# Kernel optimization log

Hardware: AMD Instinct MI355X
Metric: run time of the kernel (lower is better)

The kernel has to match this reference:

```python
import jax, jax.numpy as jnp
import numpy as np

SCALING = 16.0 / 8.0  # lora_alpha / r


def setup_inputs() -> dict:
    key = jax.random.key(0)
    k1, k2, k3, k4 = jax.random.split(key, 4)
    B, S, D_IN, D_OUT, R = 4, 4096, 4096, 4096, 8
    x = jax.random.normal(k1, (B, S, D_IN), dtype=jnp.float32)
    weight = jax.random.normal(k2, (D_OUT, D_IN), dtype=jnp.float32) * 0.02
    lora_A = jax.random.normal(k3, (R, D_IN), dtype=jnp.float32) * 0.02
    lora_B = jax.random.normal(k4, (D_OUT, R), dtype=jnp.float32) * 0.02
    return {"x": x, "weight": weight, "lora_A": lora_A, "lora_B": lora_B}


def reference(x, weight, lora_A, lora_B):
    # Base frozen linear: x @ W^T   (bias='none')
    base = jnp.einsum('bsd,od->bso', x, weight)
    # LoRA path (dropout in eval mode = identity):
    # down-project to rank r, up-project to out, scale, residual-add.
    lora_low = jnp.einsum('bsd,rd->bsr', x, lora_A)      # [B,S,r]
    lora_out = jnp.einsum('bsr,or->bso', lora_low, lora_B)  # [B,S,out]
    return base + lora_out * SCALING
```

## Files before the change

### kernel.cpp

```cpp
#include <hip/hip_runtime.h>
#include <hip/hip_bf16.h>


typedef __bf16 bf16;
typedef bf16 bf16x8 __attribute__((ext_vector_type(8)));
typedef float f32x4 __attribute__((ext_vector_type(4)));

typedef __attribute__((address_space(1))) const void* as1cv;
typedef __attribute__((address_space(3))) void* as3v;

constexpr int Mdim = 16384;
constexpr int Ndim = 4096;
constexpr int Kdim = 4096;
constexpr int Rdim = 8;
constexpr float kScale = 2.0f;

__device__ __forceinline__ unsigned short f2bf(float f) {
  union { float f; unsigned u; } v; v.f = f;
  unsigned u = v.u;
  u += 0x7fffu + ((u >> 16) & 1u);
  return (unsigned short)(u >> 16);
}

__global__ void cast_x_kernel(const float4* __restrict__ x4,
                              ushort4* __restrict__ o4, int n4) {
  int i = blockIdx.x * blockDim.x + threadIdx.x;
  int stride = gridDim.x * blockDim.x;
  for (; i < n4; i += stride) {
    float4 v = x4[i];
    ushort4 o;
    o.x = f2bf(v.x); o.y = f2bf(v.y); o.z = f2bf(v.z); o.w = f2bf(v.w);
    o4[i] = o;
  }
}

__global__ void make_weff_kernel(const float* __restrict__ W,
                                 const float* __restrict__ A,
                                 const float* __restrict__ Bm,
                                 ushort* __restrict__ weff) {
  int tid = blockIdx.x * blockDim.x + threadIdx.x;
  int kc = tid & 511;
  int n = tid >> 9;
  if (n >= Ndim) return;

  const float* wp = W + (long)n * Kdim + kc * 8;
  float4 w0 = *(const float4*)(wp);
  float4 w1 = *(const float4*)(wp + 4);

  float4 b0 = *(const float4*)(Bm + n * Rdim);
  float4 b1 = *(const float4*)(Bm + n * Rdim + 4);
  float bs[8] = {b0.x, b0.y, b0.z, b0.w, b1.x, b1.y, b1.z, b1.w};

  float l[8] = {0.f, 0.f, 0.f, 0.f, 0.f, 0.f, 0.f, 0.f};
#pragma unroll
  for (int r = 0; r < Rdim; ++r) {
    const float* ap = A + (long)r * Kdim + kc * 8;
    float4 a0 = *(const float4*)(ap);
    float4 a1 = *(const float4*)(ap + 4);
    l[0] += bs[r] * a0.x; l[1] += bs[r] * a0.y;
    l[2] += bs[r] * a0.z; l[3] += bs[r] * a0.w;
    l[4] += bs[r] * a1.x; l[5] += bs[r] * a1.y;
    l[6] += bs[r] * a1.z; l[7] += bs[r] * a1.w;
  }

  float o[8] = {w0.x + kScale * l[0], w0.y + kScale * l[1],
                w0.z + kScale * l[2], w0.w + kScale * l[3],
                w1.x + kScale * l[4], w1.y + kScale * l[5],
                w1.z + kScale * l[6], w1.w + kScale * l[7]};
  uint4 pk;
  pk.x = (unsigned)f2bf(o[0]) | ((unsigned)f2bf(o[1]) << 16);
  pk.y = (unsigned)f2bf(o[2]) | ((unsigned)f2bf(o[3]) << 16);
  pk.z = (unsigned)f2bf(o[4]) | ((unsigned)f2bf(o[5]) << 16);
  pk.w = (unsigned)f2bf(o[6]) | ((unsigned)f2bf(o[7]) << 16);
  *(uint4*)(weff + (long)n * Kdim + kc * 8) = pk;
}

#define BM 256
#define BN 256
#define BK 64
#define NT (Kdim / BK)

#define SCHED0 __builtin_amdgcn_sched_barrier(0)
#define BAR do { SCHED0; __builtin_amdgcn_s_barrier(); SCHED0; } while (0)
#define VMCNT(n) do { asm volatile("s_waitcnt vmcnt(" #n ")" ::: "memory"); SCHED0; } while (0)
#define LGKM(n) do { asm volatile("s_waitcnt lgkmcnt(" #n ")" ::: "memory"); SCHED0; } while (0)
#define GLOAD(src, dst) \
  __builtin_amdgcn_global_load_lds((as1cv)(src), (as3v)(dst), 16, 0, 0)


__global__ __launch_bounds__(512, 2) void gemm256(const bf16* __restrict__ Xb,
                                                  const bf16* __restrict__ Wb,
                                                  float* __restrict__ C) {
  __shared__ bf16 lds[2][2][2][128 * 64];

  const int tid = threadIdx.x;
  const int lane = tid & 63;
  const int wave = tid >> 6;
  const int wr = wave >> 2;
  const int wc = wave & 3;
  const int fr = lane & 15;
  const int fq = lane >> 4;

  const int wg = blockIdx.x;
  const int swz = (wg & 7) * 128 + (wg >> 3);
  const int by = swz >> 4;
  const int bx = swz & 15;
  const int brow = by * BM;
  const int bcol = bx * BN;

  const int sLow = tid >> 3;
  const int cg = (tid & 7) ^ (sLow & 7);
  const bf16* pA = Xb + (long)(brow + sLow) * Kdim + cg * 8;
  const bf16* pB =
      Wb + (long)(bcol + (sLow & 31) + (sLow >> 5) * 64) * Kdim + cg * 8;

#define STAGE_A(buf, h, kt) do {                                              \
    const bf16* s_ = pA + (long)((h) * 64) * Kdim + (((kt) & (NT - 1)) * 64); \
    GLOAD(s_, &lds[buf][0][h][0] + tid * 8);                                  \
    GLOAD(s_ + (long)128 * Kdim, &lds[buf][0][h][4096] + tid * 8);            \
  } while (0)
#define STAGE_B(buf, h, kt) do {                                              \
    const bf16* s_ = pB + (long)((h) * 32) * Kdim + (((kt) & (NT - 1)) * 64); \
    GLOAD(s_, &lds[buf][1][h][0] + tid * 8);                                  \
    GLOAD(s_ + (long)128 * Kdim, &lds[buf][1][h][4096] + tid * 8);            \
  } while (0)

  const bf16* aBs[2] = {&lds[0][0][0][(wr * 64 + fr) * 64],
                        &lds[1][0][0][(wr * 64 + fr) * 64]};
  const bf16* bBs[2] = {&lds[0][1][0][(wc * 32 + fr) * 64],
                        &lds[1][1][0][(wc * 32 + fr) * 64]};
  const int cofs0 = ((fq + 0) ^ (fr & 7)) * 8;
  const int cofs1 = ((fq + 4) ^ (fr & 7)) * 8;

  f32x4 acc[8][4];
#pragma unroll
  for (int m = 0; m < 8; ++m)
#pragma unroll
    for (int n = 0; n < 4; ++n)
      acc[m][n] = (f32x4){0.f, 0.f, 0.f, 0.f};

  bf16x8 aF[4][2];
  bf16x8 bF[2][2][2];

#define LDA(buf, mh)                                                          \
  { _Pragma("unroll") for (int m4 = 0; m4 < 4; ++m4) {                        \
      aF[m4][0] = *(const bf16x8*)(aBs[buf] + (mh) * 8192 + m4 * 1024 + cofs0); \
      aF[m4][1] = *(const bf16x8*)(aBs[buf] + (mh) * 8192 + m4 * 1024 + cofs1); \
  } }
#define LDB(buf, nh)                                                          \
  { _Pragma("unroll") for (int n2 = 0; n2 < 2; ++n2) {                        \
      bF[nh][n2][0] = *(const bf16x8*)(bBs[buf] + (nh) * 8192 + n2 * 1024 + cofs0); \
      bF[nh][n2][1] = *(const bf16x8*)(bBs[buf] + (nh) * 8192 + n2 * 1024 + cofs1); \
  } }
#define MFMAQ(mh, nh)                                                         \
  { __builtin_amdgcn_s_setprio(1);                                            \
    _Pragma("unroll") for (int m4 = 0; m4 < 4; ++m4)                          \
    _Pragma("unroll") for (int n2 = 0; n2 < 2; ++n2)                          \
    _Pragma("unroll") for (int kk = 0; kk < 2; ++kk)                          \
      acc[(mh) * 4 + m4][(nh) * 2 + n2] =                                     \
          __builtin_amdgcn_mfma_f32_16x16x32_bf16(                            \
              aF[m4][kk], bF[nh][n2][kk], acc[(mh) * 4 + m4][(nh) * 2 + n2],  \
              0, 0, 0);                                                       \
    __builtin_amdgcn_s_setprio(0); }

#define TILE(bc, bn, t) do {                                                  \
                                                                      \
    STAGE_A(bn, 1, (t) + 1);                                                  \
    LDB(bc, 1);                                                               \
    BAR; LGKM(4);                                                             \
    MFMAQ(0, 0); BAR;                                                         \
                                                                      \
    STAGE_A(bc, 0, (t) + 2);                                                  \
    BAR; LGKM(0);                                                             \
    MFMAQ(0, 1); BAR;                                                         \
                                                                      \
    LDA(bc, 1);                                                               \
    STAGE_B(bc, 0, (t) + 2);                                                  \
    BAR; LGKM(0);                                                             \
    MFMAQ(1, 1);                                                              \
    VMCNT(6); BAR;                                                            \
                                                                      \
    MFMAQ(1, 0);                                                              \
    LDA(bn, 0);                                                               \
    LDB(bn, 0);                                                               \
    STAGE_B(bc, 1, (t) + 2);                                                  \
    VMCNT(6); BAR;                                                            \
  } while (0)

  STAGE_A(0, 0, 0); STAGE_B(0, 0, 0); STAGE_B(0, 1, 0); STAGE_A(0, 1, 0);
  STAGE_A(1, 0, 1); STAGE_B(1, 0, 1); STAGE_B(1, 1, 1);
  VMCNT(6); BAR;
  LDA(0, 0);
  LDB(0, 0);

#pragma unroll 1
  for (int t = 0; t < NT; t += 2) {
    TILE(0, 1, t);
    TILE(1, 0, t + 1);
  }
  VMCNT(0);

  const int crow = brow + wr * 128 + fq * 4;
  const int ccol = bcol + wc * 64 + fr;
#pragma unroll
  for (int m = 0; m < 8; ++m) {
#pragma unroll
    for (int n = 0; n < 4; ++n) {
      f32x4 v = acc[m][n];
      long base = (long)(crow + m * 16) * Ndim + (ccol + n * 16);
      C[base] = v[0];
      C[base + Ndim] = v[1];
      C[base + 2 * (long)Ndim] = v[2];
      C[base + 3 * (long)Ndim] = v[3];
    }
  }
}

extern "C" void kernel_launch(void* const* d_in, const int* in_sizes, int n_in,
                              void* d_out, int out_size, void* d_ws,
                              size_t ws_size, hipStream_t stream) {
  const float* x = (const float*)d_in[0];
  const float* W = (const float*)d_in[1];
  const float* lA = (const float*)d_in[2];
  const float* lB = (const float*)d_in[3];
  float* out = (float*)d_out;

  ushort* xb = (ushort*)d_ws;
  ushort* weff = xb + (size_t)Mdim * Kdim;

  cast_x_kernel<<<2048, 256, 0, stream>>>((const float4*)x, (ushort4*)xb,
                                          (Mdim * Kdim) / 4);
  make_weff_kernel<<<(Ndim * (Kdim / 8)) / 256, 256, 0, stream>>>(W, lA, lB,
                                                                  weff);
  dim3 grid((Mdim / BM) * (Ndim / BN));
  gemm256<<<grid, 512, 0, stream>>>((const bf16*)xb, (const bf16*)weff, out);
}
```

Measured before the change: 564.8 us.

## Double-buffer A fragments in registers and relax scheduling barriers

```diff
diff --git a/kernel.cpp b/kernel.cpp
--- a/kernel.cpp
+++ b/kernel.cpp
@@ -81,8 +81,8 @@
 #define NT (Kdim / BK)
 
 #define SCHED0 __builtin_amdgcn_sched_barrier(0)
-#define BAR do { SCHED0; __builtin_amdgcn_s_barrier(); SCHED0; } while (0)
-#define VMCNT(n) do { asm volatile("s_waitcnt vmcnt(" #n ")" ::: "memory"); SCHED0; } while (0)
+#define BAR __builtin_amdgcn_s_barrier()
+#define VMCNT(n) asm volatile("s_waitcnt vmcnt(" #n ")" ::: "memory")
 #define LGKM(n) do { asm volatile("s_waitcnt lgkmcnt(" #n ")" ::: "memory"); SCHED0; } while (0)
 #define GLOAD(src, dst) \
   __builtin_amdgcn_global_load_lds((as1cv)(src), (as3v)(dst), 16, 0, 0)
@@ -139,27 +139,28 @@
     for (int n = 0; n < 4; ++n)
       acc[m][n] = (f32x4){0.f, 0.f, 0.f, 0.f};
 
-  bf16x8 aF[4][2];
+  bf16x8 aF0[4][2];
+  bf16x8 aF1[4][2];
   bf16x8 bF[2][2][2];
 
-#define LDA(buf, mh)                                                          \
+#define LDA(dst, buf, mh)                                                     \
   { _Pragma("unroll") for (int m4 = 0; m4 < 4; ++m4) {                        \
-      aF[m4][0] = *(const bf16x8*)(aBs[buf] + (mh) * 8192 + m4 * 1024 + cofs0); \
-      aF[m4][1] = *(const bf16x8*)(aBs[buf] + (mh) * 8192 + m4 * 1024 + cofs1); \
+      dst[m4][0] = *(const bf16x8*)(aBs[buf] + (mh) * 8192 + m4 * 1024 + cofs0); \
+      dst[m4][1] = *(const bf16x8*)(aBs[buf] + (mh) * 8192 + m4 * 1024 + cofs1); \
   } }
 #define LDB(buf, nh)                                                          \
   { _Pragma("unroll") for (int n2 = 0; n2 < 2; ++n2) {                        \
       bF[nh][n2][0] = *(const bf16x8*)(bBs[buf] + (nh) * 8192 + n2 * 1024 + cofs0); \
       bF[nh][n2][1] = *(const bf16x8*)(bBs[buf] + (nh) * 8192 + n2 * 1024 + cofs1); \
   } }
-#define MFMAQ(mh, nh)                                                         \
+#define MFMAQ(areg, mh, nh)                                                   \
   { __builtin_amdgcn_s_setprio(1);                                            \
     _Pragma("unroll") for (int m4 = 0; m4 < 4; ++m4)                          \
     _Pragma("unroll") for (int n2 = 0; n2 < 2; ++n2)                          \
     _Pragma("unroll") for (int kk = 0; kk < 2; ++kk)                          \
       acc[(mh) * 4 + m4][(nh) * 2 + n2] =                                     \
           __builtin_amdgcn_mfma_f32_16x16x32_bf16(                            \
-              aF[m4][kk], bF[nh][n2][kk], acc[(mh) * 4 + m4][(nh) * 2 + n2],  \
+              areg[m4][kk], bF[nh][n2][kk], acc[(mh) * 4 + m4][(nh) * 2 + n2],\
               0, 0, 0);                                                       \
     __builtin_amdgcn_s_setprio(0); }
 
@@ -168,20 +169,20 @@
     STAGE_A(bn, 1, (t) + 1);                                                  \
     LDB(bc, 1);                                                               \
     BAR; LGKM(4);                                                             \
-    MFMAQ(0, 0); BAR;                                                         \
+    MFMAQ(aF0, 0, 0); BAR;                                                    \
                                                                       \
     STAGE_A(bc, 0, (t) + 2);                                                  \
-    BAR; LGKM(0);                                                             \
-    MFMAQ(0, 1); BAR;                                                         \
-                                                                      \
-    LDA(bc, 1);                                                               \
+    LDA(aF1, bc, 1);                                                          \
+    BAR; LGKM(8);                                                             \
+    MFMAQ(aF0, 0, 1); BAR;                                                    \
+                                                                      \
     STAGE_B(bc, 0, (t) + 2);                                                  \
     BAR; LGKM(0);                                                             \
-    MFMAQ(1, 1);                                                              \
+    MFMAQ(aF1, 1, 1);                                                         \
     VMCNT(6); BAR;                                                            \
                                                                       \
-    MFMAQ(1, 0);                                                              \
-    LDA(bn, 0);                                                               \
+    MFMAQ(aF1, 1, 0);                                                         \
+    LDA(aF0, bn, 0);                                                          \
     LDB(bn, 0);                                                               \
     STAGE_B(bc, 1, (t) + 2);                                                  \
     VMCNT(6); BAR;                                                            \
@@ -190,7 +191,7 @@
   STAGE_A(0, 0, 0); STAGE_B(0, 0, 0); STAGE_B(0, 1, 0); STAGE_A(0, 1, 0);
   STAGE_A(1, 0, 1); STAGE_B(1, 0, 1); STAGE_B(1, 1, 1);
   VMCNT(6); BAR;
-  LDA(0, 0);
+  LDA(aF0, 0, 0);
   LDB(0, 0);
 
 #pragma unroll 1
@@ -199,6 +200,7 @@
     TILE(1, 0, t + 1);
   }
   VMCNT(0);
+  LGKM(0);
 
   const int crow = brow + wr * 128 + fq * 4;
   const int ccol = bcol + wc * 64 + fr;
```

Result: no change. 567.4 us (+0.5%).
